# Kernel optimization log

Hardware: AMD Instinct MI355X
Metric: run time of the kernel (lower is better)

The kernel has to match this reference:

```python
import jax, jax.numpy as jnp
import numpy as np
from jax import lax

D = 64
ROWS, COLS = np.triu_indices(D)  # 2080 upper-triangular (row, col) pairs, row-major like the python loop
BN_S = 1.0 / np.sqrt(1.0 + 1e-5)  # inference BN with running_mean=0, running_var=1


def _bn_relu(x, g, b):
    # inference-mode BatchNorm2d (fresh running stats) followed by ReLU; x is NCHW
    return jax.nn.relu(x * (g * BN_S)[None, :, None, None] + b[None, :, None, None])


def _conv(x, w, stride, pad):
    return lax.conv_general_dilated(x, w, (stride, stride), [(pad, pad), (pad, pad)],
                                    dimension_numbers=('NCHW', 'OIHW', 'NCHW'))


def _block(x, g1, b1, w1, g2, b2, w2, stride, ws=None):
    xa = _bn_relu(x, g1, b1)
    y = _conv(xa, w1, stride, 1)
    y = _conv(_bn_relu(y, g2, b2), w2, 1, 1)
    sc = xa if ws is None else _conv(xa, ws, stride, 0)
    return y + sc


def _forward(x, y, conv_w, s1_g1, s1_b1, s1_w1, s1_g2, s1_b2, s1_w2,
             s2_g1, s2_b1, s2_w1, s2_g2, s2_b2, s2_w2, s2_ws,
             s3_g1, s3_b1, s3_w1, s3_g2, s3_b2, s3_w2, s3_ws,
             bn_g, bn_b, ct_w, ct_b):
    h = _conv(x, conv_w, 1, 1)                                   # (B,16,36,60)
    h = _block(h, s1_g1, s1_b1, s1_w1, s1_g2, s1_b2, s1_w2, 1)    # (B,16,36,60)
    h = _block(h, s2_g1, s2_b1, s2_w1, s2_g2, s2_b2, s2_w2, 2, s2_ws)  # (B,32,18,30)
    h = _block(h, s3_g1, s3_b1, s3_w1, s3_g2, s3_b2, s3_w2, 2, s3_ws)  # (B,64,9,15)
    h = _bn_relu(h, bn_g, bn_b)                                   # (B,64,9,15)
    xp = jnp.transpose(h, (0, 2, 3, 1))                           # (B,9,15,64) channels-last
    # triangular bilinear pooling: z[..., k] = x[..., row_k] * x[..., col_k]
    z = xp[..., ROWS] * xp[..., COLS]                             # (B,9,15,2080)
    # 1x1 conv d2 -> 64 ("condtoc") + channel gating
    A = jnp.einsum('bhwk,ok->bhwo', z, ct_w) + ct_b               # (B,9,15,64)
    G = jnp.mean(A, axis=(1, 2), keepdims=True)                   # (B,1,1,64) adaptive avg pool
    Dg = A * G + A
    out = xp * Dg + xp                                            # (B,9,15,64)
    return out


def setup_inputs() -> dict:
    key = jax.random.key(0)
    ks = iter(jax.random.split(key, 40))

    def rn(shape, scale=0.1):
        return jax.random.normal(next(ks), shape, dtype=jnp.float32) * scale

    def gm(shape):
        return jax.random.uniform(next(ks), shape, dtype=jnp.float32, minval=0.5, maxval=1.5)

    return {
        'x': rn((64, 3, 36, 60), 1.0), 'y': rn((64, 2), 1.0),
        'conv_w': rn((16, 3, 3, 3)),
        's1_g1': gm((16,)), 's1_b1': rn((16,)), 's1_w1': rn((16, 16, 3, 3)),
        's1_g2': gm((16,)), 's1_b2': rn((16,)), 's1_w2': rn((16, 16, 3, 3)),
        's2_g1': gm((16,)), 's2_b1': rn((16,)), 's2_w1': rn((32, 16, 3, 3)),
        's2_g2': gm((32,)), 's2_b2': rn((32,)), 's2_w2': rn((32, 32, 3, 3)),
        's2_ws': rn((32, 16, 1, 1)),
        's3_g1': gm((32,)), 's3_b1': rn((32,)), 's3_w1': rn((64, 32, 3, 3)),
        's3_g2': gm((64,)), 's3_b2': rn((64,)), 's3_w2': rn((64, 64, 3, 3)),
        's3_ws': rn((64, 32, 1, 1)),
        'bn_g': gm((64,)), 'bn_b': rn((64,)),
        'ct_w': rn((64, 2080), 0.02), 'ct_b': rn((64,), 0.02),
    }


def reference(x, y, conv_w, s1_g1, s1_b1, s1_w1, s1_g2, s1_b2, s1_w2,
              s2_g1, s2_b1, s2_w1, s2_g2, s2_b2, s2_w2, s2_ws,
              s3_g1, s3_b1, s3_w1, s3_g2, s3_b2, s3_w2, s3_ws,
              bn_g, bn_b, ct_w, ct_b):
    return _forward(x, y, conv_w, s1_g1, s1_b1, s1_w1, s1_g2, s1_b2, s1_w2,
                    s2_g1, s2_b1, s2_w1, s2_g2, s2_b2, s2_w2, s2_ws,
                    s3_g1, s3_b1, s3_w1, s3_g2, s3_b2, s3_w2, s3_ws,
                    bn_g, bn_b, ct_w, ct_b)
```

## Files before the change

### kernel.cpp

```cpp
#include <hip/hip_runtime.h>

#define BN_S 0.9999950000374997f

constexpr int BATCH = 64;

typedef __attribute__((ext_vector_type(8))) short bf16x8;
typedef __attribute__((ext_vector_type(4))) float f32x4;

__device__ __forceinline__ float bnrelu(float x, float gs, float bb) {
    return fmaxf(fmaf(x, gs, bb), 0.f);
}

__device__ __forceinline__ unsigned short f2bf(float f) {
    unsigned u = __builtin_bit_cast(unsigned, f);
    return (unsigned short)((u + 0x7FFFu + ((u >> 16) & 1u)) >> 16);
}
__device__ __forceinline__ float bf2f(unsigned short h) {
    unsigned u = ((unsigned)h) << 16;
    return __builtin_bit_cast(float, u);
}

template<int CIN, int CICH, int COUT, int CO_PER, int HIN, int WIN,
         int HOUT, int WOUT, int STRIDE, int ROWS, int P, int PARTS,
         bool PRE_BN, int SC, int CSC, int SSTR, int SCPARTS>
__global__ __launch_bounds__(256) void convT_k(
    const float* __restrict__ in, size_t in_pstride,
    const float* __restrict__ w,
    const float* __restrict__ g, const float* __restrict__ bb,
    const float* __restrict__ xin, size_t xin_pstride,
    const float* __restrict__ g1v, const float* __restrict__ b1v,
    const float* __restrict__ wsc,
    float* __restrict__ out, size_t out_pstride)
{
    constexpr int IR = (STRIDE == 1) ? ROWS + 2 : 2 * ROWS + 1;
    constexpr int TW = (STRIDE == 1) ? WIN + 2 : WIN + 1;
    constexpr int AW = (P - 1) * STRIDE + 3;
    constexpr int NCOG = COUT / CO_PER;
    constexpr int PGW = WOUT / P;
    constexpr int NG = ROWS * PGW;
    constexpr int NITEMS = NG * NCOG;

    __shared__ float xs[CICH * IR * TW];
    __shared__ float wlds[CICH * 9 * COUT];
    __shared__ float g1l[SC ? CSC : 1], b1l[SC ? CSC : 1];
    __shared__ float wscl[(SC == 2) ? CSC * COUT : 1];

    const int band = blockIdx.x, b = blockIdx.y, zci = blockIdx.z;
    const int ci0 = zci * CICH;
    const int r0 = band * ROWS;
    const int r0in = r0 * STRIDE - 1;
    const int tid = threadIdx.x;

    for (int i = tid; i < CICH * 9 * COUT; i += 256) {
        int co = i % COUT; int rem = i / COUT; int tap = rem % 9; int ci = rem / 9;
        wlds[i] = w[((size_t)co * CIN + ci0 + ci) * 9 + tap];
    }
    if constexpr (SC != 0) {
        if (tid < CSC) { g1l[tid] = g1v[tid] * BN_S; b1l[tid] = b1v[tid]; }
        if constexpr (SC == 2) {
            for (int i = tid; i < CSC * COUT; i += 256) {
                int co = i % COUT; int ci = i / COUT;
                wscl[i] = wsc[(size_t)co * CSC + ci];
            }
        }
    }
    for (int i = tid; i < CICH * IR * TW; i += 256) {
        int cc = i % TW; int rem = i / TW; int rr = rem % IR; int ci = rem / IR;
        int gr = r0in + rr; int gc = cc - 1;
        float v = 0.f;
        if (gr >= 0 && gr < HIN && gc >= 0 && gc < WIN) {
            size_t off = ((size_t)(b * CIN + ci0 + ci) * HIN + gr) * WIN + gc;
            v = in[off];
            if constexpr (PARTS >= 2) v += in[off + in_pstride];
            if constexpr (PARTS >= 3) v += in[off + 2 * in_pstride];
            if constexpr (PARTS >= 4) v += in[off + 3 * in_pstride];
            if constexpr (PRE_BN) v = bnrelu(v, g[ci0 + ci] * BN_S, bb[ci0 + ci]);
        }
        xs[i] = v;
    }
    __syncthreads();

    for (int it = tid; it < NITEMS; it += 256) {
        const int cog = it / NG; const int gi = it % NG;
        const int lr = gi / PGW; const int wc = (gi % PGW) * P;
        float acc[P][CO_PER];
#pragma unroll
        for (int j = 0; j < P; ++j)
#pragma unroll
            for (int co = 0; co < CO_PER; ++co) acc[j][co] = 0.f;

        for (int ci = 0; ci < CICH; ++ci) {
            const float* xb = xs + ((ci * IR) + lr * STRIDE) * TW + wc * STRIDE;
#pragma unroll
            for (int dh = 0; dh < 3; ++dh) {
                float aw[AW];
#pragma unroll
                for (int a = 0; a < AW; ++a) aw[a] = xb[dh * TW + a];
#pragma unroll
                for (int dw = 0; dw < 3; ++dw) {
                    const float* wp = wlds + (ci * 9 + dh * 3 + dw) * COUT + cog * CO_PER;
#pragma unroll
                    for (int c4 = 0; c4 < CO_PER; c4 += 4) {
                        float4 wv = *(const float4*)(wp + c4);
#pragma unroll
                        for (int j = 0; j < P; ++j) {
                            float a_ = aw[j * STRIDE + dw];
                            acc[j][c4 + 0] = fmaf(a_, wv.x, acc[j][c4 + 0]);
                            acc[j][c4 + 1] = fmaf(a_, wv.y, acc[j][c4 + 1]);
                            acc[j][c4 + 2] = fmaf(a_, wv.z, acc[j][c4 + 2]);
                            acc[j][c4 + 3] = fmaf(a_, wv.w, acc[j][c4 + 3]);
                        }
                    }
                }
            }
        }

        if constexpr (SC == 1) {
            if (zci == 0) {
#pragma unroll
                for (int co = 0; co < CO_PER; ++co) {
                    int c = cog * CO_PER + co;
#pragma unroll
                    for (int j = 0; j < P; ++j) {
                        size_t off = ((size_t)(b * CSC + c) * HOUT + (r0 + lr)) * WOUT + wc + j;
                        float v = xin[off];
#pragma unroll
                        for (int s = 1; s < SCPARTS; ++s) v += xin[off + s * xin_pstride];
                        acc[j][co] += bnrelu(v, g1l[c], b1l[c]);
                    }
                }
            }
        }
        if constexpr (SC == 2) {
            if (zci == 0) {
                const int hix = (r0 + lr) * SSTR;
                for (int ci = 0; ci < CSC; ++ci) {
                    float vv[P];
#pragma unroll
                    for (int j = 0; j < P; ++j) {
                        size_t off = ((size_t)(b * CSC + ci) * (HOUT * SSTR) + hix) * (WOUT * SSTR)
                                     + (wc + j) * SSTR;
                        float v = xin[off];
#pragma unroll
                        for (int s = 1; s < SCPARTS; ++s) v += xin[off + s * xin_pstride];
                        vv[j] = bnrelu(v, g1l[ci], b1l[ci]);
                    }
                    const float* wp = wscl + ci * COUT + cog * CO_PER;
#pragma unroll
                    for (int c4 = 0; c4 < CO_PER; c4 += 4) {
                        float4 wv = *(const float4*)(wp + c4);
#pragma unroll
                        for (int j = 0; j < P; ++j) {
                            acc[j][c4 + 0] = fmaf(vv[j], wv.x, acc[j][c4 + 0]);
                            acc[j][c4 + 1] = fmaf(vv[j], wv.y, acc[j][c4 + 1]);
                            acc[j][c4 + 2] = fmaf(vv[j], wv.z, acc[j][c4 + 2]);
                            acc[j][c4 + 3] = fmaf(vv[j], wv.w, acc[j][c4 + 3]);
                        }
                    }
                }
            }
        }

        float* op = out + (size_t)zci * out_pstride
                    + ((size_t)(b * COUT + cog * CO_PER) * HOUT + (r0 + lr)) * WOUT + wc;
#pragma unroll
        for (int co = 0; co < CO_PER; ++co)
#pragma unroll
            for (int j = 0; j < P; ++j)
                op[(size_t)co * HOUT * WOUT + j] = acc[j][co];
    }
}

__global__ void f0_k(const float* __restrict__ ctw, short* __restrict__ wf)
{
    int id = blockIdx.x * 256 + threadIdx.x;
    int j = id & 7; int lane = (id >> 3) & 63; int tile = (id >> 9) & 3; int s = id >> 11;
    int c, ch;
    if (s < 32) { c = s; ch = 0; }
    else { c = 32 + ((s - 32) >> 1); ch = (s - 32) & 1; }
    int k = ch * 32 + ((lane >> 4) << 3) + j;
    int o = tile * 16 + (lane & 15);
    float val = 0.f;
    if (k <= c) val = ctw[o * 2080 + (k * (129 - k)) / 2 + (c - k)];
    wf[id] = (short)f2bf(val);
}

__global__ __launch_bounds__(256) void red_k(
    const float* __restrict__ pb, const float* __restrict__ h2,
    const float* __restrict__ g1, const float* __restrict__ b1,
    const float* __restrict__ wsc, const float* __restrict__ bng,
    const float* __restrict__ bnb, float* __restrict__ xp)
{
    __shared__ float hsc[32][136];
    __shared__ float wscl[32][16];
    __shared__ float g1l[32], b1l[32];
    const int b = blockIdx.x, cq = blockIdx.y;
    const int c0 = cq * 16;
    const int t = threadIdx.x;

    if (t < 32) { g1l[t] = g1[t] * BN_S; b1l[t] = b1[t]; }
    for (int i = t; i < 512; i += 256) {
        int ci = i & 31, cc = i >> 5;
        wscl[ci][cc] = wsc[(size_t)(c0 + cc) * 32 + ci];
    }
    __syncthreads();
    for (int i = t; i < 32 * 135; i += 256) {
        int ci = i / 135, p = i % 135;
        int hp = p / 15, wp = p % 15;
        size_t off = ((size_t)(b * 32 + ci) * 18 + hp * 2) * 30 + wp * 2;
        float v = h2[off] + h2[off + 1105920] + h2[off + 2 * 1105920] + h2[off + 3 * 1105920];
        hsc[ci][p] = bnrelu(v, g1l[ci], b1l[ci]);
    }
    __syncthreads();

    for (int e = t; e < 16 * 135; e += 256) {
        int cc = e / 135, p = e % 135;
        int c = c0 + cc;
        size_t idx = ((size_t)(b * 64 + c)) * 135 + p;
        float y = 0.f;
#pragma unroll
        for (int q = 0; q < 8; ++q) y += pb[idx + (size_t)q * 552960];
#pragma unroll 8
        for (int ci = 0; ci < 32; ++ci) y = fmaf(hsc[ci][p], wscl[ci][cc], y);
        xp[((size_t)b * 135 + p) * 64 + c] = bnrelu(y, bng[c] * BN_S, bnb[c]);
    }
}

template<int NCH>
__device__ __forceinline__ void f2m_body(
    const unsigned short* xs, int q, const short* __restrict__ wf,
    const float* __restrict__ ctb, float* __restrict__ Abase, int p0, int t)
{
    float* A = Abase + (size_t)q * 552960;
    const int w = t >> 6, lane = t & 63;
    const int prow = w * 32;
    const int lrow = lane & 15, lk = lane >> 4;

    bf16x8 Af[2][NCH];
#pragma unroll
    for (int rt = 0; rt < 2; ++rt)
#pragma unroll
        for (int ch = 0; ch < NCH; ++ch) {
            int pix = prow + rt * 16 + lrow;
            int g = ch * 4 + lk;
            Af[rt][ch] = *(const bf16x8*)&xs[pix * 64 + ((g ^ (pix & 7)) * 8)];
        }

    f32x4 acc[2][4];
#pragma unroll
    for (int rt = 0; rt < 2; ++rt)
#pragma unroll
        for (int tt = 0; tt < 4; ++tt) acc[rt][tt] = f32x4{0.f, 0.f, 0.f, 0.f};

    const int c0 = q * 16;
    bf16x8 BA[NCH][4], BB[NCH][4];

    auto loadB = [&](int c, bf16x8 (&B)[NCH][4]) {
        int slotb = (NCH == 1) ? c : (2 * c - 32);
#pragma unroll
        for (int ch = 0; ch < NCH; ++ch) {
            const short* wb = wf + (size_t)(slotb + ch) * 2048 + lane * 8;
#pragma unroll
            for (int tt = 0; tt < 4; ++tt)
                B[ch][tt] = *(const bf16x8*)(wb + tt * 512);
        }
    };
    auto compute = [&](int c, bf16x8 (&B)[NCH][4]) {
        f32x4 S[2][4];
#pragma unroll
        for (int rt = 0; rt < 2; ++rt)
#pragma unroll
            for (int tt = 0; tt < 4; ++tt) S[rt][tt] = f32x4{0.f, 0.f, 0.f, 0.f};
#pragma unroll
        for (int ch = 0; ch < NCH; ++ch)
#pragma unroll
            for (int tt = 0; tt < 4; ++tt) {
                S[0][tt] = __builtin_amdgcn_mfma_f32_16x16x32_bf16(Af[0][ch], B[ch][tt], S[0][tt], 0, 0, 0);
                S[1][tt] = __builtin_amdgcn_mfma_f32_16x16x32_bf16(Af[1][ch], B[ch][tt], S[1][tt], 0, 0, 0);
            }
#pragma unroll
        for (int rt = 0; rt < 2; ++rt)
#pragma unroll
            for (int j = 0; j < 4; ++j) {
                int pix = prow + rt * 16 + lk * 4 + j;
                float sv = bf2f(xs[pix * 64 + (((c >> 3) ^ (pix & 7)) * 8) + (c & 7)]);
#pragma unroll
                for (int tt = 0; tt < 4; ++tt)
                    acc[rt][tt][j] += sv * S[rt][tt][j];
            }
    };

    loadB(c0, BA);
#pragma unroll 1
    for (int ci = 0; ci < 16; ci += 2) {
        loadB(c0 + ci + 1, BB);
        compute(c0 + ci, BA);
        if (ci < 14) loadB(c0 + ci + 2, BA);
        compute(c0 + ci + 1, BB);
    }

#pragma unroll
    for (int rt = 0; rt < 2; ++rt)
#pragma unroll
        for (int j = 0; j < 4; ++j) {
            int gpix = p0 + prow + rt * 16 + lk * 4 + j;
            if (gpix < 8640) {
#pragma unroll
                for (int tt = 0; tt < 4; ++tt) {
                    int o = tt * 16 + lrow;
                    float vv = acc[rt][tt][j];
                    if (q == 0) vv += ctb[o];
                    A[(size_t)gpix * 64 + o] = vv;
                }
            }
        }
}

__global__ __launch_bounds__(256) void f2m_k(
    const float* __restrict__ xp, const short* __restrict__ wf,
    const float* __restrict__ ctb, float* __restrict__ Abase)
{
    __shared__ unsigned short xs[128 * 64];
    const int t = threadIdx.x;
    const int p0 = blockIdx.x * 128;
    const int q = blockIdx.y;

    {
        int pr = t >> 1, h = t & 1;
        int gp = p0 + pr;
        float v[32];
        if (gp < 8640) {
            const float4* src = (const float4*)(xp + (size_t)gp * 64 + h * 32);
#pragma unroll
            for (int i = 0; i < 8; ++i) {
                float4 x4 = src[i];
                v[i*4+0] = x4.x; v[i*4+1] = x4.y; v[i*4+2] = x4.z; v[i*4+3] = x4.w;
            }
        } else {
#pragma unroll
            for (int i = 0; i < 32; ++i) v[i] = 0.f;
        }
#pragma unroll
        for (int g = 0; g < 4; ++g) {
            unsigned w0 = f2bf(v[g*8+0]) | ((unsigned)f2bf(v[g*8+1]) << 16);
            unsigned w1 = f2bf(v[g*8+2]) | ((unsigned)f2bf(v[g*8+3]) << 16);
            unsigned w2 = f2bf(v[g*8+4]) | ((unsigned)f2bf(v[g*8+5]) << 16);
            unsigned w3 = f2bf(v[g*8+6]) | ((unsigned)f2bf(v[g*8+7]) << 16);
            int grp = h * 4 + g;
            int sg = grp ^ (pr & 7);
            *(uint4*)&xs[pr * 64 + sg * 8] = make_uint4(w0, w1, w2, w3);
        }
    }
    __syncthreads();

    if (q < 2) f2m_body<1>(xs, q, wf, ctb, Abase, p0, t);
    else       f2m_body<2>(xs, q, wf, ctb, Abase, p0, t);
}

__global__ void f3a_k(const float* __restrict__ A, float* __restrict__ G)
{
    int b = blockIdx.x; int t = threadIdx.x;
    int o = t & 63; int grp = t >> 6;
    float s = 0.f;
    for (int p = grp; p < 135; p += 4) {
        size_t off = ((size_t)b * 135 + p) * 64 + o;
        s += A[off] + A[off + 552960] + A[off + 2 * 552960] + A[off + 3 * 552960];
    }
    __shared__ float red[4][64];
    red[grp][o] = s;
    __syncthreads();
    if (t < 64) G[b * 64 + t] = (red[0][t] + red[1][t] + red[2][t] + red[3][t]) * (1.0f / 135.0f);
}

__global__ void f3b_k(const float* __restrict__ xp, const float* __restrict__ A,
                      const float* __restrict__ G, float* __restrict__ out)
{
    int idx = blockIdx.x * 256 + threadIdx.x;
    if (idx >= BATCH * 135 * 64) return;
    int o = idx & 63; int b = idx / (135 * 64);
    float a = A[idx] + A[idx + 552960] + A[idx + 2 * 552960] + A[idx + 3 * 552960];
    float g = G[b * 64 + o];
    float x = xp[idx];
    out[idx] = fmaf(x, a * (g + 1.f), x);
}

extern "C" void kernel_launch(void* const* d_in, const int* in_sizes, int n_in,
                              void* d_out, int out_size, void* d_ws, size_t ws_size,
                              hipStream_t stream)
{
    const float* x      = (const float*)d_in[0];
    const float* conv_w = (const float*)d_in[2];
    const float* s1_g1  = (const float*)d_in[3];
    const float* s1_b1  = (const float*)d_in[4];
    const float* s1_w1  = (const float*)d_in[5];
    const float* s1_g2  = (const float*)d_in[6];
    const float* s1_b2  = (const float*)d_in[7];
    const float* s1_w2  = (const float*)d_in[8];
    const float* s2_g1  = (const float*)d_in[9];
    const float* s2_b1  = (const float*)d_in[10];
    const float* s2_w1  = (const float*)d_in[11];
    const float* s2_g2  = (const float*)d_in[12];
    const float* s2_b2  = (const float*)d_in[13];
    const float* s2_w2  = (const float*)d_in[14];
    const float* s2_ws  = (const float*)d_in[15];
    const float* s3_g1  = (const float*)d_in[16];
    const float* s3_b1  = (const float*)d_in[17];
    const float* s3_w1  = (const float*)d_in[18];
    const float* s3_g2  = (const float*)d_in[19];
    const float* s3_b2  = (const float*)d_in[20];
    const float* s3_w2  = (const float*)d_in[21];
    const float* s3_ws  = (const float*)d_in[22];
    const float* bn_g   = (const float*)d_in[23];
    const float* bn_b   = (const float*)d_in[24];
    const float* ct_w   = (const float*)d_in[25];
    const float* ct_b   = (const float*)d_in[26];
    float* out = (float*)d_out;

    float* ws = (float*)d_ws;
    float* h0      = ws + 0;
    float* p_b1c1  = ws + 2211840;
    float* h1      = ws + 11059200;
    float* p_b2c1  = ws + 0;
    float* p_b2c2  = ws + 4423680;
    float* p_b3c1  = ws + 0;
    float* p_b3c2  = ws + 8847360;
    float* xp      = ws + 0;
    float* A       = ws + 552960;
    float* G       = ws + 15482880;
    short* wfrag   = (short*)(ws + 15487232);

    dim3 blk(256);

    f0_k<<<768, blk, 0, stream>>>(ct_w, wfrag);

    convT_k<3, 3, 16, 8, 36, 60, 36, 60, 1, 6, 3, 1, false, 0, 1, 1, 1>
        <<<dim3(6, 64, 1), blk, 0, stream>>>(
        x, 0, conv_w, nullptr, nullptr, nullptr, 0, nullptr, nullptr, nullptr, h0, 0);
    convT_k<16, 4, 16, 8, 36, 60, 36, 60, 1, 9, 5, 1, true, 0, 1, 1, 1>
        <<<dim3(4, 64, 4), blk, 0, stream>>>(
        h0, 0, s1_w1, s1_g1, s1_b1, nullptr, 0, nullptr, nullptr, nullptr, p_b1c1, 2211840);
    convT_k<16, 8, 16, 8, 36, 60, 36, 60, 1, 9, 5, 4, true, 1, 16, 1, 1>
        <<<dim3(4, 64, 2), blk, 0, stream>>>(
        p_b1c1, 2211840, s1_w2, s1_g2, s1_b2, h0, 0, s1_g1, s1_b1, nullptr, h1, 2211840);
    convT_k<16, 4, 32, 8, 36, 60, 18, 30, 2, 6, 5, 2, true, 0, 1, 1, 1>
        <<<dim3(3, 64, 4), blk, 0, stream>>>(
        h1, 2211840, s2_w1, s2_g1, s2_b1, nullptr, 0, nullptr, nullptr, nullptr, p_b2c1, 1105920);
    convT_k<32, 8, 32, 8, 18, 30, 18, 30, 1, 6, 5, 4, true, 2, 16, 2, 2>
        <<<dim3(3, 64, 4), blk, 0, stream>>>(
        p_b2c1, 1105920, s2_w2, s2_g2, s2_b2, h1, 2211840, s2_g1, s2_b1, s2_ws, p_b2c2, 1105920);
    convT_k<32, 8, 64, 4, 18, 30, 9, 15, 2, 3, 3, 4, true, 0, 1, 1, 1>
        <<<dim3(3, 64, 4), blk, 0, stream>>>(
        p_b2c2, 1105920, s3_w1, s3_g1, s3_b1, nullptr, 0, nullptr, nullptr, nullptr, p_b3c1, 552960);
    convT_k<64, 8, 64, 4, 9, 15, 9, 15, 1, 3, 3, 4, true, 0, 1, 1, 1>
        <<<dim3(3, 64, 8), blk, 0, stream>>>(
        p_b3c1, 552960, s3_w2, s3_g2, s3_b2, nullptr, 0, nullptr, nullptr, nullptr, p_b3c2, 552960);
    red_k<<<dim3(64, 4), blk, 0, stream>>>(p_b3c2, p_b2c2,
                                           s3_g1, s3_b1, s3_ws, bn_g, bn_b, xp);
    f2m_k<<<dim3(68, 4), blk, 0, stream>>>(xp, wfrag, ct_b, A);

    f3a_k<<<64, blk, 0, stream>>>(A, G);
    f3b_k<<<2160, blk, 0, stream>>>(xp, A, G, out);
}
```

Before: 202.7 us.

## Fuse stem conv and stage-1 block into one tiled kernel; halve split-K partials

Adds a kernel that computes the stem conv, both stage-1 convolutions with their BN/ReLU, and the residual add per 4-row band in shared memory, recomputing halo rows, and writes h1 directly. This replaces three launches and the h0 and partial-sum round trips through global memory. The remaining convolutions use larger input-channel chunks, so there are fewer split-K partial buffers and the reduction loops sum fewer partials. In exchange, the fused kernel uses heavy shared memory (about 80 KB), recomputes halo rows, and runs only 576 blocks with some threads idle.

```diff
diff --git a/kernel.cpp b/kernel.cpp
--- a/kernel.cpp
+++ b/kernel.cpp
@@ -18,6 +18,159 @@
 __device__ __forceinline__ float bf2f(unsigned short h) {
     unsigned u = ((unsigned)h) << 16;
     return __builtin_bit_cast(float, u);
+}
+
+__global__ __launch_bounds__(256) void b1f_k(
+    const float* __restrict__ x, const float* __restrict__ w0,
+    const float* __restrict__ w1, const float* __restrict__ g1v,
+    const float* __restrict__ b1v, const float* __restrict__ w2,
+    const float* __restrict__ g2v, const float* __restrict__ b2v,
+    float* __restrict__ h1)
+{
+    __shared__ float uni[5952];
+    __shared__ float h0a[7936];
+    __shared__ float wst[432], w1l[2304], w2l[2304];
+    __shared__ float g1l[16], b1l[16], g2l[16], b2l[16];
+
+    const int band = blockIdx.x, b = blockIdx.y;
+    const int R0 = band * 4;
+    const int t = threadIdx.x;
+
+    for (int i = t; i < 432; i += 256) {
+        int co = i & 15; int tap = (i >> 4) % 9; int ci = i / 144;
+        wst[i] = w0[(co * 3 + ci) * 9 + tap];
+    }
+    for (int i = t; i < 2304; i += 256) {
+        int co = i & 15; int tap = (i >> 4) % 9; int ci = i / 144;
+        w1l[i] = w1[(co * 16 + ci) * 9 + tap];
+        w2l[i] = w2[(co * 16 + ci) * 9 + tap];
+    }
+    if (t < 16) {
+        g1l[t] = g1v[t] * BN_S; b1l[t] = b1v[t];
+        g2l[t] = g2v[t] * BN_S; b2l[t] = b2v[t];
+    }
+    for (int i = t; i < 1860; i += 256) {
+        int cc = i % 62; int rr = (i / 62) % 10; int ci = i / 620;
+        int gr = R0 - 3 + rr, gc = cc - 1;
+        float v = 0.f;
+        if (gr >= 0 && gr < 36 && gc >= 0 && gc < 60)
+            v = x[((size_t)(b * 3 + ci) * 36 + gr) * 60 + gc];
+        uni[i] = v;
+    }
+    __syncthreads();
+
+    for (int it = t; it < 384; it += 256) {
+        const int cog = it / 96; int rem = it % 96;
+        const int r = rem / 12; const int wc = (rem % 12) * 5;
+        const int gr = R0 - 2 + r;
+        float acc[5][4] = {};
+        if (gr >= 0 && gr < 36) {
+            for (int ci = 0; ci < 3; ++ci) {
+#pragma unroll
+                for (int dh = 0; dh < 3; ++dh) {
+                    float aw[7];
+#pragma unroll
+                    for (int a = 0; a < 7; ++a) aw[a] = uni[(ci * 10 + r + dh) * 62 + wc + a];
+#pragma unroll
+                    for (int dw = 0; dw < 3; ++dw) {
+                        const float* wp = wst + (ci * 9 + dh * 3 + dw) * 16 + cog * 4;
+#pragma unroll
+                        for (int c = 0; c < 4; ++c)
+#pragma unroll
+                            for (int j = 0; j < 5; ++j)
+                                acc[j][c] = fmaf(aw[j + dw], wp[c], acc[j][c]);
+                    }
+                }
+            }
+        }
+#pragma unroll
+        for (int c = 0; c < 4; ++c) {
+            int co = cog * 4 + c;
+#pragma unroll
+            for (int j = 0; j < 5; ++j) {
+                float v = (gr >= 0 && gr < 36) ? bnrelu(acc[j][c], g1l[co], b1l[co]) : 0.f;
+                h0a[(co * 8 + r) * 62 + wc + 1 + j] = v;
+            }
+        }
+    }
+    if (t < 256) {
+        int co = t & 15; int r = (t >> 4) & 7; int e = t >> 7;
+        h0a[(co * 8 + r) * 62 + (e ? 61 : 0)] = 0.f;
+    }
+    __syncthreads();
+
+    for (int it = t; it < 288; it += 256) {
+        const int cog = it / 72; int rem = it % 72;
+        const int r = rem / 12; const int wc = (rem % 12) * 5;
+        const int gr = R0 - 1 + r;
+        float acc[5][4] = {};
+        if (gr >= 0 && gr < 36) {
+            for (int ci = 0; ci < 16; ++ci) {
+#pragma unroll
+                for (int dh = 0; dh < 3; ++dh) {
+                    float aw[7];
+#pragma unroll
+                    for (int a = 0; a < 7; ++a) aw[a] = h0a[(ci * 8 + r + dh) * 62 + wc + a];
+#pragma unroll
+                    for (int dw = 0; dw < 3; ++dw) {
+                        const float* wp = w1l + (ci * 9 + dh * 3 + dw) * 16 + cog * 4;
+#pragma unroll
+                        for (int c = 0; c < 4; ++c)
+#pragma unroll
+                            for (int j = 0; j < 5; ++j)
+                                acc[j][c] = fmaf(aw[j + dw], wp[c], acc[j][c]);
+                    }
+                }
+            }
+        }
+#pragma unroll
+        for (int c = 0; c < 4; ++c) {
+            int co = cog * 4 + c;
+#pragma unroll
+            for (int j = 0; j < 5; ++j) {
+                float v = (gr >= 0 && gr < 36) ? bnrelu(acc[j][c], g2l[co], b2l[co]) : 0.f;
+                uni[(co * 6 + r) * 62 + wc + 1 + j] = v;
+            }
+        }
+    }
+    if (t < 192) {
+        int co = t & 15; int rem = t >> 4; int r = rem % 6; int e = rem / 6;
+        uni[(co * 6 + r) * 62 + (e ? 61 : 0)] = 0.f;
+    }
+    __syncthreads();
+
+    for (int it = t; it < 192; it += 256) {
+        const int cog = it / 48; int rem = it % 48;
+        const int r = rem / 12; const int wc = (rem % 12) * 5;
+        const int gr = R0 + r;
+        float acc[5][4] = {};
+        for (int ci = 0; ci < 16; ++ci) {
+#pragma unroll
+            for (int dh = 0; dh < 3; ++dh) {
+                float aw[7];
+#pragma unroll
+                for (int a = 0; a < 7; ++a) aw[a] = uni[(ci * 6 + r + dh) * 62 + wc + a];
+#pragma unroll
+                for (int dw = 0; dw < 3; ++dw) {
+                    const float* wp = w2l + (ci * 9 + dh * 3 + dw) * 16 + cog * 4;
+#pragma unroll
+                    for (int c = 0; c < 4; ++c)
+#pragma unroll
+                        for (int j = 0; j < 5; ++j)
+                            acc[j][c] = fmaf(aw[j + dw], wp[c], acc[j][c]);
+                }
+            }
+        }
+#pragma unroll
+        for (int c = 0; c < 4; ++c) {
+            int co = cog * 4 + c;
+#pragma unroll
+            for (int j = 0; j < 5; ++j) {
+                float v = acc[j][c] + h0a[(co * 8 + r + 2) * 62 + wc + 1 + j];
+                h1[((size_t)(b * 16 + co) * 36 + gr) * 60 + wc + j] = v;
+            }
+        }
+    }
 }
 
 template<int CIN, int CICH, int COUT, int CO_PER, int HIN, int WIN,
@@ -208,7 +361,7 @@
         int ci = i / 135, p = i % 135;
         int hp = p / 15, wp = p % 15;
         size_t off = ((size_t)(b * 32 + ci) * 18 + hp * 2) * 30 + wp * 2;
-        float v = h2[off] + h2[off + 1105920] + h2[off + 2 * 1105920] + h2[off + 3 * 1105920];
+        float v = h2[off] + h2[off + 1105920];
         hsc[ci][p] = bnrelu(v, g1l[ci], b1l[ci]);
     }
     __syncthreads();
@@ -219,7 +372,7 @@
         size_t idx = ((size_t)(b * 64 + c)) * 135 + p;
         float y = 0.f;
 #pragma unroll
-        for (int q = 0; q < 8; ++q) y += pb[idx + (size_t)q * 552960];
+        for (int q = 0; q < 4; ++q) y += pb[idx + (size_t)q * 552960];
 #pragma unroll 8
         for (int ci = 0; ci < 32; ++ci) y = fmaf(hsc[ci][p], wscl[ci][cc], y);
         xp[((size_t)b * 135 + p) * 64 + c] = bnrelu(y, bng[c] * BN_S, bnb[c]);
@@ -417,42 +570,33 @@
     float* out = (float*)d_out;
 
     float* ws = (float*)d_ws;
-    float* h0      = ws + 0;
-    float* p_b1c1  = ws + 2211840;
-    float* h1      = ws + 11059200;
-    float* p_b2c1  = ws + 0;
+    float* h1      = ws + 0;
+    float* p_b2c1  = ws + 2211840;
     float* p_b2c2  = ws + 4423680;
-    float* p_b3c1  = ws + 0;
-    float* p_b3c2  = ws + 8847360;
-    float* xp      = ws + 0;
-    float* A       = ws + 552960;
-    float* G       = ws + 15482880;
-    short* wfrag   = (short*)(ws + 15487232);
+    float* p_b3c1  = ws + 6635520;
+    float* p_b3c2  = ws + 7741440;
+    float* xp      = ws + 9953280;
+    float* A       = ws + 10506240;
+    float* G       = ws + 12718080;
+    short* wfrag   = (short*)(ws + 12722176);
 
     dim3 blk(256);
 
     f0_k<<<768, blk, 0, stream>>>(ct_w, wfrag);
 
-    convT_k<3, 3, 16, 8, 36, 60, 36, 60, 1, 6, 3, 1, false, 0, 1, 1, 1>
-        <<<dim3(6, 64, 1), blk, 0, stream>>>(
-        x, 0, conv_w, nullptr, nullptr, nullptr, 0, nullptr, nullptr, nullptr, h0, 0);
-    convT_k<16, 4, 16, 8, 36, 60, 36, 60, 1, 9, 5, 1, true, 0, 1, 1, 1>
-        <<<dim3(4, 64, 4), blk, 0, stream>>>(
-        h0, 0, s1_w1, s1_g1, s1_b1, nullptr, 0, nullptr, nullptr, nullptr, p_b1c1, 2211840);
-    convT_k<16, 8, 16, 8, 36, 60, 36, 60, 1, 9, 5, 4, true, 1, 16, 1, 1>
-        <<<dim3(4, 64, 2), blk, 0, stream>>>(
-        p_b1c1, 2211840, s1_w2, s1_g2, s1_b2, h0, 0, s1_g1, s1_b1, nullptr, h1, 2211840);
-    convT_k<16, 4, 32, 8, 36, 60, 18, 30, 2, 6, 5, 2, true, 0, 1, 1, 1>
+    b1f_k<<<dim3(9, 64), blk, 0, stream>>>(
+        x, conv_w, s1_w1, s1_g1, s1_b1, s1_w2, s1_g2, s1_b2, h1);
+    convT_k<16, 8, 32, 4, 36, 60, 18, 30, 2, 6, 5, 1, true, 0, 1, 1, 1>
+        <<<dim3(3, 64, 2), blk, 0, stream>>>(
+        h1, 0, s2_w1, s2_g1, s2_b1, nullptr, 0, nullptr, nullptr, nullptr, p_b2c1, 1105920);
+    convT_k<32, 16, 32, 4, 18, 30, 18, 30, 1, 6, 5, 2, true, 2, 16, 2, 1>
+        <<<dim3(3, 64, 2), blk, 0, stream>>>(
+        p_b2c1, 1105920, s2_w2, s2_g2, s2_b2, h1, 0, s2_g1, s2_b1, s2_ws, p_b2c2, 1105920);
+    convT_k<32, 16, 64, 4, 18, 30, 9, 15, 2, 3, 3, 2, true, 0, 1, 1, 1>
+        <<<dim3(3, 64, 2), blk, 0, stream>>>(
+        p_b2c2, 1105920, s3_w1, s3_g1, s3_b1, nullptr, 0, nullptr, nullptr, nullptr, p_b3c1, 552960);
+    convT_k<64, 16, 64, 4, 9, 15, 9, 15, 1, 3, 3, 2, true, 0, 1, 1, 1>
         <<<dim3(3, 64, 4), blk, 0, stream>>>(
-        h1, 2211840, s2_w1, s2_g1, s2_b1, nullptr, 0, nullptr, nullptr, nullptr, p_b2c1, 1105920);
-    convT_k<32, 8, 32, 8, 18, 30, 18, 30, 1, 6, 5, 4, true, 2, 16, 2, 2>
-        <<<dim3(3, 64, 4), blk, 0, stream>>>(
-        p_b2c1, 1105920, s2_w2, s2_g2, s2_b2, h1, 2211840, s2_g1, s2_b1, s2_ws, p_b2c2, 1105920);
-    convT_k<32, 8, 64, 4, 18, 30, 9, 15, 2, 3, 3, 4, true, 0, 1, 1, 1>
-        <<<dim3(3, 64, 4), blk, 0, stream>>>(
-        p_b2c2, 1105920, s3_w1, s3_g1, s3_b1, nullptr, 0, nullptr, nullptr, nullptr, p_b3c1, 552960);
-    convT_k<64, 8, 64, 4, 9, 15, 9, 15, 1, 3, 3, 4, true, 0, 1, 1, 1>
-        <<<dim3(3, 64, 8), blk, 0, stream>>>(
         p_b3c1, 552960, s3_w2, s3_g2, s3_b2, nullptr, 0, nullptr, nullptr, nullptr, p_b3c2, 552960);
     red_k<<<dim3(64, 4), blk, 0, stream>>>(p_b3c2, p_b2c2,
                                            s3_g1, s3_b1, s3_ws, bn_g, bn_b, xp);
```

Measured after the change: 228.3 us. 12.6% more time.
